# Kernel optimization log

Hardware: AMD Instinct MI355X
Metric: run time of the kernel (lower is better)

The kernel has to match this reference:

```python
import jax, jax.numpy as jnp
import numpy as np

B, C, H, W = 8, 128, 256, 256
D = 64            # embed_dim
S = 32            # max_segments


def setup_inputs() -> dict:
    key = jax.random.key(0)
    ks = jax.random.split(key, 8)
    return {
        "segment_labels": jax.random.randint(ks[0], (B, 1, H, W), 0, S, dtype=jnp.int32),
        "features": jax.random.normal(ks[1], (B, C, H, W), jnp.float32),
        # 1x1 conv stack feat_proj: Conv2d(C->D), ReLU, Conv2d(D->D)
        "conv1_w": jax.random.normal(ks[2], (D, C), jnp.float32) * 0.05,
        "conv1_b": jnp.zeros((D,), jnp.float32),
        "conv2_w": jax.random.normal(ks[3], (D, D), jnp.float32) * 0.1,
        "conv2_b": jnp.zeros((D,), jnp.float32),
        # nn.Embedding(max_segments + 1, embed_dim)
        "embed_table": jax.random.normal(ks[4], (S + 1, D), jnp.float32) * 0.02,
        # nn.Linear(2*D, D): y = x @ W.T + b, W is (out, in)
        "out_w": jax.random.normal(ks[5], (D, 2 * D), jnp.float32) * 0.05,
        "out_b": jnp.zeros((D,), jnp.float32),
    }


def reference(segment_labels, features, conv1_w, conv1_b, conv2_w, conv2_b,
              embed_table, out_w, out_b):
    Bb, Cc, Hh, Ww = features.shape
    P = Hh * Ww
    Smax = embed_table.shape[0] - 1  # max_segments

    # feat_proj: two 1x1 convs == per-pixel GEMMs
    x = features.reshape(Bb, Cc, P)                                   # (B,C,P)
    h1 = jnp.maximum(jnp.einsum('oc,bcp->bpo', conv1_w, x) + conv1_b, 0.0)  # (B,P,D)
    feat = jnp.einsum('od,bpd->bpo', conv2_w, h1) + conv2_b           # (B,P,D)

    # Per-(batch, segment-id) masked mean via a single segment-sum pass.
    labels = segment_labels[:, 0].reshape(Bb, P)                       # (B,P) in [0,S)
    ids = (labels + Smax * jnp.arange(Bb, dtype=labels.dtype)[:, None]).reshape(-1)
    sums = jax.ops.segment_sum(feat.reshape(Bb * P, -1), ids,
                               num_segments=Bb * Smax).reshape(Bb, Smax, -1)
    counts = jax.ops.segment_sum(jnp.ones((Bb * P,), feat.dtype), ids,
                                 num_segments=Bb * Smax).reshape(Bb, Smax)
    pooled = sums / jnp.maximum(counts, 1.0)[..., None]                # (B,S,D) (zeros where absent)

    # type embedding for seg_id s (already in [0,S), clamp is a no-op but faithful)
    type_emb = embed_table[jnp.clip(jnp.arange(Smax), 0, Smax)]        # (S,D)
    combined = jnp.concatenate(
        [pooled, jnp.broadcast_to(type_emb, (Bb, Smax, type_emb.shape[-1]))], axis=-1)
    combined = jnp.einsum('oe,bse->bso', out_w, combined) + out_b      # (B,S,D)

    # torch.unique returns sorted present labels; compact present segments to the
    # front (rank order), pad rest with zeros.
    present = counts > 0                                               # (B,S)
    rank = jnp.cumsum(present.astype(jnp.int32), axis=1) - 1
    dst = jnp.where(present, rank, Smax)                               # Smax = dropped slot
    bidx = jnp.broadcast_to(jnp.arange(Bb)[:, None], (Bb, Smax))
    out = jnp.zeros_like(combined)
    out = out.at[bidx, dst].set(combined, mode='drop')
    return out
```

## Files before the change

kernel.cpp:

```cpp
#include <hip/hip_runtime.h>


#define B_ 8
#define C_ 128
#define P_ 65536
#define D_ 64
#define S_ 32
#define TM 256
#define KC 32
#define NCH (C_ / KC)

typedef short  bf16x8 __attribute__((ext_vector_type(8)));
typedef float  f32x4  __attribute__((ext_vector_type(4)));

__device__ __forceinline__ short f2bf(float f) {
  union { float f; unsigned u; } v; v.f = f;
  unsigned r = v.u + 0x7fffu + ((v.u >> 16) & 1u);
  return (short)(r >> 16);
}

__device__ __forceinline__ void gload16(const float* g, float* l) {
  __builtin_amdgcn_global_load_lds(
      (const __attribute__((address_space(1))) void*)g,
      (__attribute__((address_space(3))) void*)l, 16, 0, 0);
}

__global__ __launch_bounds__(256) void w1_to_bf16(const float* __restrict__ w1,
                                                  short* __restrict__ wbf) {
  int i = blockIdx.x * 256 + threadIdx.x;
  if (i < C_ * D_) wbf[i] = f2bf(w1[i]);
}

__global__ __launch_bounds__(256, 2) void proj_mfma(
    const int* __restrict__ labels, const float* __restrict__ feat,
    const short* __restrict__ wbf, const float* __restrict__ b1,
    float* __restrict__ gsum, int* __restrict__ gcnt)
{
  __shared__ __align__(16) float lds_x[2][KC * TM];
  __shared__ float s_acc[S_][68];
  __shared__ int   s_cnt[S_];

  const int tid  = threadIdx.x;
  const int wave = tid >> 6, l = tid & 63, m = l & 15, g = l >> 4;
  const int b    = blockIdx.y;
  const int px0  = blockIdx.x * TM;

  for (int i = tid; i < S_ * 68; i += 256) ((float*)s_acc)[i] = 0.f;
  if (tid < S_) s_cnt[tid] = 0;
  __syncthreads();

  const float* xb = feat + (size_t)b * C_ * P_ + px0;
  const int lane4 = l * 4;

  #pragma unroll
  for (int i = 0; i < 8; ++i)
    gload16(xb + (size_t)(wave * 8 + i) * P_ + lane4,
            &lds_x[0][(wave * 8 + i) * TM]);

  f32x4 acc[4][4];
  #pragma unroll
  for (int t = 0; t < 4; ++t)
    #pragma unroll
    for (int nt = 0; nt < 4; ++nt) acc[t][nt] = (f32x4){0.f, 0.f, 0.f, 0.f};

  #pragma unroll
  for (int kc = 0; kc < NCH; ++kc) {
    bf16x8 bw[4];
    #pragma unroll
    for (int nt = 0; nt < 4; ++nt)
      bw[nt] = *(const bf16x8*)&wbf[(nt * 16 + m) * C_ + kc * KC + g * 8];

    if (kc + 1 < NCH) {
      #pragma unroll
      for (int i = 0; i < 8; ++i)
        gload16(xb + (size_t)((kc + 1) * KC + wave * 8 + i) * P_ + lane4,
                &lds_x[(kc + 1) & 1][(wave * 8 + i) * TM]);
      asm volatile("s_waitcnt vmcnt(8)" ::: "memory");
    } else {
      asm volatile("s_waitcnt vmcnt(0)" ::: "memory");
    }
    __builtin_amdgcn_s_barrier();
    asm volatile("" ::: "memory");

    const float* bp = lds_x[kc & 1];
    #pragma unroll
    for (int t = 0; t < 4; ++t) {
      const int bpx = wave * 64 + t * 16 + m;
      bf16x8 af;
      #pragma unroll
      for (int j = 0; j < 8; ++j)
        af[j] = f2bf(bp[(g * 8 + j) * TM + bpx]);
      #pragma unroll
      for (int nt = 0; nt < 4; ++nt)
        acc[t][nt] = __builtin_amdgcn_mfma_f32_16x16x32_bf16(af, bw[nt],
                                                             acc[t][nt], 0, 0, 0);
    }
    asm volatile("s_waitcnt lgkmcnt(0)" ::: "memory");
    __builtin_amdgcn_sched_barrier(0);
    __builtin_amdgcn_s_barrier();
  }

  float b1v[4];
  #pragma unroll
  for (int nt = 0; nt < 4; ++nt) b1v[nt] = b1[nt * 16 + m];

  const int* lb = labels + (size_t)b * P_ + px0;
  #pragma unroll
  for (int t = 0; t < 4; ++t) {
    const int4 lv = *(const int4*)&lb[wave * 64 + t * 16 + g * 4];
    #pragma unroll
    for (int nt = 0; nt < 4; ++nt) {
      #pragma unroll
      for (int r = 0; r < 4; ++r) {
        const int lab = ((r & 2) ? ((r & 1) ? lv.w : lv.z)
                                 : ((r & 1) ? lv.y : lv.x)) & (S_ - 1);
        const float v = fmaxf(acc[t][nt][r] + b1v[nt], 0.f);
        atomicAdd(&s_acc[lab][nt * 16 + m], v);
      }
    }
    if (m < 4) {
      const int lab = ((m & 2) ? ((m & 1) ? lv.w : lv.z)
                               : ((m & 1) ? lv.y : lv.x)) & (S_ - 1);
      atomicAdd(&s_cnt[lab], 1);
    }
  }

  __syncthreads();
  for (int i = tid; i < S_ * D_; i += 256)
    atomicAdd(&gsum[(size_t)b * S_ * D_ + i], s_acc[i >> 6][i & 63]);
  if (tid < S_) atomicAdd(&gcnt[b * S_ + tid], s_cnt[tid]);
}

__global__ __launch_bounds__(64) void seg_finalize2(
    const float* __restrict__ gsum, const int* __restrict__ gcnt,
    const float* __restrict__ w2, const float* __restrict__ b2,
    const float* __restrict__ emb, const float* __restrict__ wo,
    const float* __restrict__ bo, float* __restrict__ out)
{
  const int s = blockIdx.x, b = blockIdx.y, o = threadIdx.x;
  const int co = (o < S_) ? gcnt[b * S_ + o] : 0;
  const unsigned long long mask = __ballot(co > 0);
  const int cnt = gcnt[b * S_ + s];
  if (cnt <= 0) return;
  const int rank = __popcll(mask & ((1ull << s) - 1ull));

  __shared__ float s_mean[D_], s_pool[D_];
  s_mean[o] = gsum[((size_t)b * S_ + s) * D_ + o] * (1.f / (float)cnt);
  __syncthreads();
  float pooled = b2[o];
  #pragma unroll
  for (int d = 0; d < D_; ++d) pooled += w2[o * D_ + d] * s_mean[d];
  s_pool[o] = pooled;
  __syncthreads();
  float r = bo[o];
  #pragma unroll
  for (int e = 0; e < D_; ++e) r += wo[o * 2 * D_ + e] * s_pool[e];
  #pragma unroll
  for (int e = 0; e < D_; ++e) r += wo[o * 2 * D_ + D_ + e] * emb[s * D_ + e];
  out[((size_t)b * S_ + rank) * D_ + o] = r;
}

extern "C" void kernel_launch(void* const* d_in, const int* in_sizes, int n_in,
                              void* d_out, int out_size, void* d_ws, size_t ws_size,
                              hipStream_t stream) {
  const int*   labels = (const int*)  d_in[0];
  const float* feat   = (const float*)d_in[1];
  const float* w1     = (const float*)d_in[2];
  const float* b1     = (const float*)d_in[3];
  const float* w2     = (const float*)d_in[4];
  const float* b2     = (const float*)d_in[5];
  const float* emb    = (const float*)d_in[6];
  const float* wo     = (const float*)d_in[7];
  const float* bo     = (const float*)d_in[8];
  float* out = (float*)d_out;

  char* w = (char*)d_ws;
  float* gsum = (float*)w;   w += (size_t)B_ * S_ * D_ * 4;
  int*   gcnt = (int*)w;     w += (size_t)B_ * S_ * 4;
  short* wbf  = (short*)w;

  hipMemsetAsync(d_ws, 0, (size_t)B_ * S_ * D_ * 4 + (size_t)B_ * S_ * 4, stream);
  hipMemsetAsync(d_out, 0, (size_t)out_size * sizeof(float), stream);

  w1_to_bf16<<<(C_ * D_ + 255) / 256, 256, 0, stream>>>(w1, wbf);

  dim3 grid(P_ / TM, B_);
  proj_mfma<<<grid, 256, 0, stream>>>(labels, feat, wbf, b1, gsum, gcnt);
  seg_finalize2<<<dim3(S_, B_), 64, 0, stream>>>(gsum, gcnt, w2, b2, emb, wo, bo, out);
}
```

Before: 233.6 us.

## Load features directly to registers with per-wave double-buffered pipeline and swizzled LDS weights

Replaces the block-wide LDS staging of feature tiles (global_load_lds with barriers) with per-wave direct global-to-register loads, software-pipelined across two register buffers so the next 16-pixel tile is in flight while the current one runs through MFMA. The bf16 weight matrix is staged once into XOR-swizzled LDS instead of being re-read from global memory on every K chunk. Each block now covers 512 pixels, with a higher occupancy hint and no intra-loop barriers. In exchange it uses many more registers (64 floats of prefetch), and each lane's loads are strided 64-byte segments rather than wide 16-byte vectors, which may hurt memory efficiency.

```diff
diff --git a/kernel.cpp b/kernel.cpp
--- a/kernel.cpp
+++ b/kernel.cpp
@@ -6,9 +6,9 @@
 #define P_ 65536
 #define D_ 64
 #define S_ 32
-#define TM 256
-#define KC 32
-#define NCH (C_ / KC)
+#define WPB 4
+#define TMW 128
+#define TMB (WPB * TMW)
 
 typedef short  bf16x8 __attribute__((ext_vector_type(8)));
 typedef float  f32x4  __attribute__((ext_vector_type(4)));
@@ -19,111 +19,98 @@
   return (short)(r >> 16);
 }
 
-__device__ __forceinline__ void gload16(const float* g, float* l) {
-  __builtin_amdgcn_global_load_lds(
-      (const __attribute__((address_space(1))) void*)g,
-      (__attribute__((address_space(3))) void*)l, 16, 0, 0);
-}
-
 __global__ __launch_bounds__(256) void w1_to_bf16(const float* __restrict__ w1,
                                                   short* __restrict__ wbf) {
   int i = blockIdx.x * 256 + threadIdx.x;
   if (i < C_ * D_) wbf[i] = f2bf(w1[i]);
 }
 
-__global__ __launch_bounds__(256, 2) void proj_mfma(
+__global__ __launch_bounds__(256, 4) void proj_mfma(
     const int* __restrict__ labels, const float* __restrict__ feat,
     const short* __restrict__ wbf, const float* __restrict__ b1,
     float* __restrict__ gsum, int* __restrict__ gcnt)
 {
-  __shared__ __align__(16) float lds_x[2][KC * TM];
+  __shared__ __align__(16) char wlds[D_ * 256];
   __shared__ float s_acc[S_][68];
   __shared__ int   s_cnt[S_];
 
   const int tid  = threadIdx.x;
   const int wave = tid >> 6, l = tid & 63, m = l & 15, g = l >> 4;
   const int b    = blockIdx.y;
-  const int px0  = blockIdx.x * TM;
+  const int px0  = blockIdx.x * TMB;
 
+  #pragma unroll
+  for (int i = 0; i < 4; ++i) {
+    const int e = tid * 32 + i * 8;
+    const int row = e >> 7, colB = (e & 127) * 2;
+    *(bf16x8*)&wlds[row * 256 + (colB ^ ((row & 7) << 4))] =
+        *(const bf16x8*)&wbf[e];
+  }
   for (int i = tid; i < S_ * 68; i += 256) ((float*)s_acc)[i] = 0.f;
   if (tid < S_) s_cnt[tid] = 0;
   __syncthreads();
 
-  const float* xb = feat + (size_t)b * C_ * P_ + px0;
-  const int lane4 = l * 4;
-
-  #pragma unroll
-  for (int i = 0; i < 8; ++i)
-    gload16(xb + (size_t)(wave * 8 + i) * P_ + lane4,
-            &lds_x[0][(wave * 8 + i) * TM]);
-
-  f32x4 acc[4][4];
-  #pragma unroll
-  for (int t = 0; t < 4; ++t)
-    #pragma unroll
-    for (int nt = 0; nt < 4; ++nt) acc[t][nt] = (f32x4){0.f, 0.f, 0.f, 0.f};
-
-  #pragma unroll
-  for (int kc = 0; kc < NCH; ++kc) {
-    bf16x8 bw[4];
-    #pragma unroll
-    for (int nt = 0; nt < 4; ++nt)
-      bw[nt] = *(const bf16x8*)&wbf[(nt * 16 + m) * C_ + kc * KC + g * 8];
-
-    if (kc + 1 < NCH) {
-      #pragma unroll
-      for (int i = 0; i < 8; ++i)
-        gload16(xb + (size_t)((kc + 1) * KC + wave * 8 + i) * P_ + lane4,
-                &lds_x[(kc + 1) & 1][(wave * 8 + i) * TM]);
-      asm volatile("s_waitcnt vmcnt(8)" ::: "memory");
-    } else {
-      asm volatile("s_waitcnt vmcnt(0)" ::: "memory");
-    }
-    __builtin_amdgcn_s_barrier();
-    asm volatile("" ::: "memory");
-
-    const float* bp = lds_x[kc & 1];
-    #pragma unroll
-    for (int t = 0; t < 4; ++t) {
-      const int bpx = wave * 64 + t * 16 + m;
-      bf16x8 af;
-      #pragma unroll
-      for (int j = 0; j < 8; ++j)
-        af[j] = f2bf(bp[(g * 8 + j) * TM + bpx]);
-      #pragma unroll
-      for (int nt = 0; nt < 4; ++nt)
-        acc[t][nt] = __builtin_amdgcn_mfma_f32_16x16x32_bf16(af, bw[nt],
-                                                             acc[t][nt], 0, 0, 0);
-    }
-    asm volatile("s_waitcnt lgkmcnt(0)" ::: "memory");
-    __builtin_amdgcn_sched_barrier(0);
-    __builtin_amdgcn_s_barrier();
-  }
+  const float* xpg = feat + (size_t)b * C_ * P_ + (size_t)(g * 8) * P_
+                   + px0 + wave * TMW + m;
+  const int*   lb  = labels + (size_t)b * P_ + px0 + wave * TMW;
+  const int    xsw = (m & 7) << 4;
 
   float b1v[4];
   #pragma unroll
   for (int nt = 0; nt < 4; ++nt) b1v[nt] = b1[nt * 16 + m];
 
-  const int* lb = labels + (size_t)b * P_ + px0;
+  float xvA[4][8], xvB[4][8];
+
+#define ISSUE(dst, t_) do {                                                   \
+    _Pragma("unroll") for (int kk = 0; kk < 4; ++kk)                          \
+    _Pragma("unroll") for (int j = 0; j < 8; ++j)                             \
+      dst[kk][j] = xpg[(size_t)(kk * 32 + j) * P_ + (t_) * 16];               \
+  } while (0)
+
+#define COMPUTE(src, t_) do {                                                 \
+    f32x4 acc[4] = {{0,0,0,0},{0,0,0,0},{0,0,0,0},{0,0,0,0}};                 \
+    _Pragma("unroll") for (int ks = 0; ks < 4; ++ks) {                        \
+      bf16x8 af;                                                              \
+      _Pragma("unroll") for (int j = 0; j < 8; ++j) af[j] = f2bf(src[ks][j]); \
+      _Pragma("unroll") for (int nt = 0; nt < 4; ++nt) {                      \
+        bf16x8 bwv = *(const bf16x8*)&wlds[(nt * 16 + m) * 256 +              \
+                                           ((ks * 64 + g * 16) ^ xsw)];       \
+        acc[nt] = __builtin_amdgcn_mfma_f32_16x16x32_bf16(af, bwv,            \
+                                                          acc[nt], 0, 0, 0);  \
+      }                                                                       \
+    }                                                                         \
+    const int4 lv = *(const int4*)&lb[(t_) * 16 + g * 4];                     \
+    _Pragma("unroll") for (int nt = 0; nt < 4; ++nt)                          \
+      _Pragma("unroll") for (int r = 0; r < 4; ++r) {                         \
+        const int lab = ((r & 2) ? ((r & 1) ? lv.w : lv.z)                    \
+                                 : ((r & 1) ? lv.y : lv.x)) & (S_ - 1);       \
+        atomicAdd(&s_acc[lab][nt * 16 + m],                                   \
+                  fmaxf(acc[nt][r] + b1v[nt], 0.f));                          \
+      }                                                                       \
+    if (m < 4) {                                                              \
+      const int lab = ((m & 2) ? ((m & 1) ? lv.w : lv.z)                      \
+                               : ((m & 1) ? lv.y : lv.x)) & (S_ - 1);         \
+      atomicAdd(&s_cnt[lab], 1);                                              \
+    }                                                                         \
+  } while (0)
+
+  ISSUE(xvA, 0);
+  __builtin_amdgcn_sched_barrier(0);
   #pragma unroll
-  for (int t = 0; t < 4; ++t) {
-    const int4 lv = *(const int4*)&lb[wave * 64 + t * 16 + g * 4];
-    #pragma unroll
-    for (int nt = 0; nt < 4; ++nt) {
-      #pragma unroll
-      for (int r = 0; r < 4; ++r) {
-        const int lab = ((r & 2) ? ((r & 1) ? lv.w : lv.z)
-                                 : ((r & 1) ? lv.y : lv.x)) & (S_ - 1);
-        const float v = fmaxf(acc[t][nt][r] + b1v[nt], 0.f);
-        atomicAdd(&s_acc[lab][nt * 16 + m], v);
-      }
+  for (int t = 0; t < 8; t += 2) {
+    ISSUE(xvB, t + 1);
+    __builtin_amdgcn_sched_barrier(0);
+    COMPUTE(xvA, t);
+    __builtin_amdgcn_sched_barrier(0);
+    if (t + 2 < 8) {
+      ISSUE(xvA, t + 2);
+      __builtin_amdgcn_sched_barrier(0);
     }
-    if (m < 4) {
-      const int lab = ((m & 2) ? ((m & 1) ? lv.w : lv.z)
-                               : ((m & 1) ? lv.y : lv.x)) & (S_ - 1);
-      atomicAdd(&s_cnt[lab], 1);
-    }
+    COMPUTE(xvB, t + 1);
+    __builtin_amdgcn_sched_barrier(0);
   }
+#undef ISSUE
+#undef COMPUTE
 
   __syncthreads();
   for (int i = tid; i < S_ * D_; i += 256)
@@ -184,7 +171,7 @@
 
   w1_to_bf16<<<(C_ * D_ + 255) / 256, 256, 0, stream>>>(w1, wbf);
 
-  dim3 grid(P_ / TM, B_);
+  dim3 grid(P_ / TMB, B_);
   proj_mfma<<<grid, 256, 0, stream>>>(labels, feat, wbf, b1, gsum, gcnt);
   seg_finalize2<<<dim3(S_, B_), 64, 0, stream>>>(gsum, gcnt, w2, b2, emb, wo, bo, out);
 }
```

Result: faster. 203.4 us (-12.9%).

## Replace double buffer with 4-stage padded LDS ring and preload weights

Applied to the files above, without the earlier changes.

The projection kernel's two-slot 32-channel double buffer becomes a four-slot ring of 16-channel stages, with up to four stages in flight and rows padded to 260 floats to reduce LDS bank conflicts. All bf16 weight fragments and biases are loaded into registers once before the loop, and the K loop is fully unrolled into four explicit phases with hand-placed waits and barriers. The goal is deeper prefetch of the memory-bound feature stream and fewer per-chunk weight loads, at the cost of more registers and more fragile hand scheduling.

```diff
diff --git a/kernel.cpp b/kernel.cpp
--- a/kernel.cpp
+++ b/kernel.cpp
@@ -6,12 +6,11 @@
 #define P_ 65536
 #define D_ 64
 #define S_ 32
-#define TM 256
-#define KC 32
-#define NCH (C_ / KC)
-
-typedef short  bf16x8 __attribute__((ext_vector_type(8)));
-typedef float  f32x4  __attribute__((ext_vector_type(4)));
+#define PXT 256
+#define ROWPAD 260
+
+typedef short bf16x8 __attribute__((ext_vector_type(8)));
+typedef float f32x4  __attribute__((ext_vector_type(4)));
 
 __device__ __forceinline__ short f2bf(float f) {
   union { float f; unsigned u; } v; v.f = f;
@@ -19,16 +18,16 @@
   return (short)(r >> 16);
 }
 
-__device__ __forceinline__ void gload16(const float* g, float* l) {
-  __builtin_amdgcn_global_load_lds(
-      (const __attribute__((address_space(1))) void*)g,
-      (__attribute__((address_space(3))) void*)l, 16, 0, 0);
-}
-
 __global__ __launch_bounds__(256) void w1_to_bf16(const float* __restrict__ w1,
                                                   short* __restrict__ wbf) {
   int i = blockIdx.x * 256 + threadIdx.x;
   if (i < C_ * D_) wbf[i] = f2bf(w1[i]);
+}
+
+__device__ __forceinline__ void gload16(const float* g, const float* l) {
+  __builtin_amdgcn_global_load_lds(
+      (const __attribute__((address_space(1))) float*)g,
+      (__attribute__((address_space(3))) float*)l, 16, 0, 0);
 }
 
 __global__ __launch_bounds__(256, 2) void proj_mfma(
@@ -36,86 +35,100 @@
     const short* __restrict__ wbf, const float* __restrict__ b1,
     float* __restrict__ gsum, int* __restrict__ gcnt)
 {
-  __shared__ __align__(16) float lds_x[2][KC * TM];
+  __shared__ __align__(16) float ring[4][16 * ROWPAD];
   __shared__ float s_acc[S_][68];
   __shared__ int   s_cnt[S_];
 
   const int tid  = threadIdx.x;
   const int wave = tid >> 6, l = tid & 63, m = l & 15, g = l >> 4;
   const int b    = blockIdx.y;
-  const int px0  = blockIdx.x * TM;
+  const int px0  = blockIdx.x * PXT;
 
   for (int i = tid; i < S_ * 68; i += 256) ((float*)s_acc)[i] = 0.f;
   if (tid < S_) s_cnt[tid] = 0;
-  __syncthreads();
+
+  bf16x8 bfr[4][4];
+  #pragma unroll
+  for (int nt = 0; nt < 4; ++nt)
+    #pragma unroll
+    for (int u = 0; u < 4; ++u)
+      bfr[nt][u] = *(const bf16x8*)&wbf[(nt * 16 + m) * C_ + u * 32 + g * 8];
+  float b1v[4];
+  #pragma unroll
+  for (int nt = 0; nt < 4; ++nt) b1v[nt] = b1[nt * 16 + m];
 
   const float* xb = feat + (size_t)b * C_ * P_ + px0;
-  const int lane4 = l * 4;
-
-  #pragma unroll
-  for (int i = 0; i < 8; ++i)
-    gload16(xb + (size_t)(wave * 8 + i) * P_ + lane4,
-            &lds_x[0][(wave * 8 + i) * TM]);
+
+#define STAGE(c_) do {                                                        \
+    _Pragma("unroll") for (int i = 0; i < 4; ++i)                             \
+      gload16(xb + (size_t)((c_) * 16 + wave * 4 + i) * P_ + l * 4,           \
+              &ring[(c_) & 3][(wave * 4 + i) * ROWPAD]);                      \
+  } while (0)
+
+#define WAITV(n_) do {                                                        \
+    asm volatile("s_waitcnt vmcnt(" #n_ ")" ::: "memory");                    \
+    __builtin_amdgcn_sched_barrier(0);                                        \
+  } while (0)
+
+#define PAIR(u_) do {                                                         \
+    _Pragma("unroll") for (int v = 0; v < 4; ++v) {                           \
+      const int px = wave * 64 + v * 16 + m;                                  \
+      const float* sl = &ring[(2 * (u_) + (g >> 1)) & 3]                      \
+                             [((g & 1) * 8) * ROWPAD + px];                   \
+      bf16x8 af;                                                              \
+      _Pragma("unroll") for (int j = 0; j < 8; ++j)                           \
+        af[j] = f2bf(sl[j * ROWPAD]);                                         \
+      _Pragma("unroll") for (int nt = 0; nt < 4; ++nt)                        \
+        acc[v][nt] = __builtin_amdgcn_mfma_f32_16x16x32_bf16(                 \
+            af, bfr[nt][u_], acc[v][nt], 0, 0, 0);                            \
+    }                                                                         \
+  } while (0)
+
+  STAGE(0); STAGE(1); STAGE(2); STAGE(3);
 
   f32x4 acc[4][4];
   #pragma unroll
-  for (int t = 0; t < 4; ++t)
+  for (int v = 0; v < 4; ++v)
     #pragma unroll
-    for (int nt = 0; nt < 4; ++nt) acc[t][nt] = (f32x4){0.f, 0.f, 0.f, 0.f};
-
-  #pragma unroll
-  for (int kc = 0; kc < NCH; ++kc) {
-    bf16x8 bw[4];
-    #pragma unroll
-    for (int nt = 0; nt < 4; ++nt)
-      bw[nt] = *(const bf16x8*)&wbf[(nt * 16 + m) * C_ + kc * KC + g * 8];
-
-    if (kc + 1 < NCH) {
-      #pragma unroll
-      for (int i = 0; i < 8; ++i)
-        gload16(xb + (size_t)((kc + 1) * KC + wave * 8 + i) * P_ + lane4,
-                &lds_x[(kc + 1) & 1][(wave * 8 + i) * TM]);
-      asm volatile("s_waitcnt vmcnt(8)" ::: "memory");
-    } else {
-      asm volatile("s_waitcnt vmcnt(0)" ::: "memory");
-    }
-    __builtin_amdgcn_s_barrier();
-    asm volatile("" ::: "memory");
-
-    const float* bp = lds_x[kc & 1];
-    #pragma unroll
-    for (int t = 0; t < 4; ++t) {
-      const int bpx = wave * 64 + t * 16 + m;
-      bf16x8 af;
-      #pragma unroll
-      for (int j = 0; j < 8; ++j)
-        af[j] = f2bf(bp[(g * 8 + j) * TM + bpx]);
-      #pragma unroll
-      for (int nt = 0; nt < 4; ++nt)
-        acc[t][nt] = __builtin_amdgcn_mfma_f32_16x16x32_bf16(af, bw[nt],
-                                                             acc[t][nt], 0, 0, 0);
-    }
-    asm volatile("s_waitcnt lgkmcnt(0)" ::: "memory");
-    __builtin_amdgcn_sched_barrier(0);
-    __builtin_amdgcn_s_barrier();
-  }
-
-  float b1v[4];
-  #pragma unroll
-  for (int nt = 0; nt < 4; ++nt) b1v[nt] = b1[nt * 16 + m];
-
-  const int* lb = labels + (size_t)b * P_ + px0;
-  #pragma unroll
-  for (int t = 0; t < 4; ++t) {
-    const int4 lv = *(const int4*)&lb[wave * 64 + t * 16 + g * 4];
+    for (int nt = 0; nt < 4; ++nt) acc[v][nt] = (f32x4){0.f, 0.f, 0.f, 0.f};
+
+  WAITV(8);
+  __builtin_amdgcn_s_barrier();
+  PAIR(0);
+  __builtin_amdgcn_sched_barrier(0);
+  __builtin_amdgcn_s_barrier();
+  STAGE(4); STAGE(5);
+  WAITV(8);
+  __builtin_amdgcn_s_barrier();
+  PAIR(1);
+  __builtin_amdgcn_sched_barrier(0);
+  __builtin_amdgcn_s_barrier();
+  STAGE(6); STAGE(7);
+  WAITV(8);
+  __builtin_amdgcn_s_barrier();
+  PAIR(2);
+  __builtin_amdgcn_sched_barrier(0);
+  WAITV(0);
+  __builtin_amdgcn_s_barrier();
+  PAIR(3);
+  __builtin_amdgcn_sched_barrier(0);
+
+#undef STAGE
+#undef WAITV
+#undef PAIR
+
+  const int* lb = labels + (size_t)b * P_ + px0 + wave * 64;
+  #pragma unroll
+  for (int v = 0; v < 4; ++v) {
+    const int4 lv = *(const int4*)&lb[v * 16 + g * 4];
     #pragma unroll
     for (int nt = 0; nt < 4; ++nt) {
       #pragma unroll
       for (int r = 0; r < 4; ++r) {
         const int lab = ((r & 2) ? ((r & 1) ? lv.w : lv.z)
                                  : ((r & 1) ? lv.y : lv.x)) & (S_ - 1);
-        const float v = fmaxf(acc[t][nt][r] + b1v[nt], 0.f);
-        atomicAdd(&s_acc[lab][nt * 16 + m], v);
+        atomicAdd(&s_acc[lab][nt * 16 + m],
+                  fmaxf(acc[v][nt][r] + b1v[nt], 0.f));
       }
     }
     if (m < 4) {
@@ -184,7 +197,7 @@
 
   w1_to_bf16<<<(C_ * D_ + 255) / 256, 256, 0, stream>>>(w1, wbf);
 
-  dim3 grid(P_ / TM, B_);
+  dim3 grid(P_ / PXT, B_);
   proj_mfma<<<grid, 256, 0, stream>>>(labels, feat, wbf, b1, gsum, gcnt);
   seg_finalize2<<<dim3(S_, B_), 64, 0, stream>>>(gsum, gcnt, w2, b2, emb, wo, bo, out);
 }
```

Result: no change. 233.0 us (-0.2%).

## Pre-convert features to bf16 and load MFMA operands directly without LDS staging

Applied to the files above, without the earlier changes.

Adds a separate pass that converts the whole fp32 feature tensor to packed bf16 in workspace, then the projection kernel reads bf16 pairs straight from global memory into MFMA A-fragments instead of staging fp32 through double-buffered LDS. Each wave now owns 128 pixels processed as two interleaved 16-pixel tiles, with all W1 fragments held in registers, and occupancy hint is raised to 4. The extra conversion pass reads 256MB and writes 128MB, so total traffic rises. The direct strided global loads may also be less coalesced than the earlier LDS path.

```diff
diff --git a/kernel.cpp b/kernel.cpp
--- a/kernel.cpp
+++ b/kernel.cpp
@@ -6,24 +6,15 @@
 #define P_ 65536
 #define D_ 64
 #define S_ 32
-#define TM 256
-#define KC 32
-#define NCH (C_ / KC)
 
-typedef short  bf16x8 __attribute__((ext_vector_type(8)));
-typedef float  f32x4  __attribute__((ext_vector_type(4)));
+typedef short bf16x8 __attribute__((ext_vector_type(8)));
+typedef float f32x4  __attribute__((ext_vector_type(4)));
 
-__device__ __forceinline__ short f2bf(float f) {
+__device__ __forceinline__ unsigned f2bfu(float f) {
   union { float f; unsigned u; } v; v.f = f;
-  unsigned r = v.u + 0x7fffu + ((v.u >> 16) & 1u);
-  return (short)(r >> 16);
+  return (v.u + 0x7fffu + ((v.u >> 16) & 1u)) >> 16;
 }
-
-__device__ __forceinline__ void gload16(const float* g, float* l) {
-  __builtin_amdgcn_global_load_lds(
-      (const __attribute__((address_space(1))) void*)g,
-      (__attribute__((address_space(3))) void*)l, 16, 0, 0);
-}
+__device__ __forceinline__ short f2bf(float f) { return (short)f2bfu(f); }
 
 __global__ __launch_bounds__(256) void w1_to_bf16(const float* __restrict__ w1,
                                                   short* __restrict__ wbf) {
@@ -31,97 +22,103 @@
   if (i < C_ * D_) wbf[i] = f2bf(w1[i]);
 }
 
-__global__ __launch_bounds__(256, 2) void proj_mfma(
-    const int* __restrict__ labels, const float* __restrict__ feat,
-    const short* __restrict__ wbf, const float* __restrict__ b1,
-    float* __restrict__ gsum, int* __restrict__ gcnt)
+__global__ __launch_bounds__(256) void feat_to_bf16(const float4* __restrict__ in,
+                                                    uint4* __restrict__ out) {
+  const int n = (B_ * C_ * P_) / 8;
+  const int stride = gridDim.x * 256;
+  for (int i = blockIdx.x * 256 + threadIdx.x; i < n; i += stride) {
+    const float4 a = in[2 * i], b = in[2 * i + 1];
+    uint4 o;
+    o.x = f2bfu(a.x) | (f2bfu(a.y) << 16);
+    o.y = f2bfu(a.z) | (f2bfu(a.w) << 16);
+    o.z = f2bfu(b.x) | (f2bfu(b.y) << 16);
+    o.w = f2bfu(b.z) | (f2bfu(b.w) << 16);
+    out[i] = o;
+  }
+}
+
+template<bool PACKED>
+__global__ __launch_bounds__(256, 4) void proj_mfma(
+    const int* __restrict__ labels, const float* __restrict__ featf,
+    const unsigned* __restrict__ featb, const short* __restrict__ wbf,
+    const float* __restrict__ b1, float* __restrict__ gsum,
+    int* __restrict__ gcnt)
 {
-  __shared__ __align__(16) float lds_x[2][KC * TM];
   __shared__ float s_acc[S_][68];
   __shared__ int   s_cnt[S_];
 
-  const int tid  = threadIdx.x;
+  const int tid = threadIdx.x;
   const int wave = tid >> 6, l = tid & 63, m = l & 15, g = l >> 4;
-  const int b    = blockIdx.y;
-  const int px0  = blockIdx.x * TM;
+  const int b   = blockIdx.y;
+  const int px0 = blockIdx.x * 512 + wave * 128;
 
   for (int i = tid; i < S_ * 68; i += 256) ((float*)s_acc)[i] = 0.f;
   if (tid < S_) s_cnt[tid] = 0;
   __syncthreads();
 
-  const float* xb = feat + (size_t)b * C_ * P_ + px0;
-  const int lane4 = l * 4;
-
+  bf16x8 bfr[4][4];
   #pragma unroll
-  for (int i = 0; i < 8; ++i)
-    gload16(xb + (size_t)(wave * 8 + i) * P_ + lane4,
-            &lds_x[0][(wave * 8 + i) * TM]);
-
-  f32x4 acc[4][4];
-  #pragma unroll
-  for (int t = 0; t < 4; ++t)
+  for (int nt = 0; nt < 4; ++nt)
     #pragma unroll
-    for (int nt = 0; nt < 4; ++nt) acc[t][nt] = (f32x4){0.f, 0.f, 0.f, 0.f};
-
-  #pragma unroll
-  for (int kc = 0; kc < NCH; ++kc) {
-    bf16x8 bw[4];
-    #pragma unroll
-    for (int nt = 0; nt < 4; ++nt)
-      bw[nt] = *(const bf16x8*)&wbf[(nt * 16 + m) * C_ + kc * KC + g * 8];
-
-    if (kc + 1 < NCH) {
-      #pragma unroll
-      for (int i = 0; i < 8; ++i)
-        gload16(xb + (size_t)((kc + 1) * KC + wave * 8 + i) * P_ + lane4,
-                &lds_x[(kc + 1) & 1][(wave * 8 + i) * TM]);
-      asm volatile("s_waitcnt vmcnt(8)" ::: "memory");
-    } else {
-      asm volatile("s_waitcnt vmcnt(0)" ::: "memory");
-    }
-    __builtin_amdgcn_s_barrier();
-    asm volatile("" ::: "memory");
-
-    const float* bp = lds_x[kc & 1];
-    #pragma unroll
-    for (int t = 0; t < 4; ++t) {
-      const int bpx = wave * 64 + t * 16 + m;
-      bf16x8 af;
-      #pragma unroll
-      for (int j = 0; j < 8; ++j)
-        af[j] = f2bf(bp[(g * 8 + j) * TM + bpx]);
-      #pragma unroll
-      for (int nt = 0; nt < 4; ++nt)
-        acc[t][nt] = __builtin_amdgcn_mfma_f32_16x16x32_bf16(af, bw[nt],
-                                                             acc[t][nt], 0, 0, 0);
-    }
-    asm volatile("s_waitcnt lgkmcnt(0)" ::: "memory");
-    __builtin_amdgcn_sched_barrier(0);
-    __builtin_amdgcn_s_barrier();
-  }
-
+    for (int ks = 0; ks < 4; ++ks)
+      bfr[nt][ks] = *(const bf16x8*)&wbf[(nt * 16 + m) * C_ + ks * 32 + g * 8];
   float b1v[4];
   #pragma unroll
   for (int nt = 0; nt < 4; ++nt) b1v[nt] = b1[nt * 16 + m];
 
-  const int* lb = labels + (size_t)b * P_ + px0;
-  #pragma unroll
-  for (int t = 0; t < 4; ++t) {
-    const int4 lv = *(const int4*)&lb[wave * 64 + t * 16 + g * 4];
+  const int* lb = labels + (size_t)b * P_;
+
+  for (int it = 0; it < 4; ++it) {
+    const int pp = px0 + it * 32;
+    f32x4 aA[4], aB[4];
     #pragma unroll
     for (int nt = 0; nt < 4; ++nt) {
+      aA[nt] = (f32x4){0.f, 0.f, 0.f, 0.f};
+      aB[nt] = (f32x4){0.f, 0.f, 0.f, 0.f};
+    }
+
+    #pragma unroll
+    for (int ks = 0; ks < 4; ++ks) {
+      bf16x8 afA, afB;
+      if (PACKED) {
+        const unsigned* xp = featb
+            + ((size_t)b * C_ + ks * 32 + g * 8) * (P_ / 2) + (pp >> 1) + m;
+        #pragma unroll
+        for (int j = 0; j < 8; ++j) {
+          const unsigned v = xp[(size_t)j * (P_ / 2)];
+          afA[j] = (short)(v & 0xffffu);
+          afB[j] = (short)(v >> 16);
+        }
+      } else {
+        const float* xp = featf
+            + ((size_t)b * C_ + ks * 32 + g * 8) * P_ + pp + 2 * m;
+        #pragma unroll
+        for (int j = 0; j < 8; ++j) {
+          afA[j] = f2bf(xp[(size_t)j * P_]);
+          afB[j] = f2bf(xp[(size_t)j * P_ + 1]);
+        }
+      }
       #pragma unroll
-      for (int r = 0; r < 4; ++r) {
-        const int lab = ((r & 2) ? ((r & 1) ? lv.w : lv.z)
-                                 : ((r & 1) ? lv.y : lv.x)) & (S_ - 1);
-        const float v = fmaxf(acc[t][nt][r] + b1v[nt], 0.f);
-        atomicAdd(&s_acc[lab][nt * 16 + m], v);
+      for (int nt = 0; nt < 4; ++nt) {
+        aA[nt] = __builtin_amdgcn_mfma_f32_16x16x32_bf16(afA, bfr[nt][ks], aA[nt], 0, 0, 0);
+        aB[nt] = __builtin_amdgcn_mfma_f32_16x16x32_bf16(afB, bfr[nt][ks], aB[nt], 0, 0, 0);
+      }
+    }
+
+    #pragma unroll
+    for (int r = 0; r < 4; ++r) {
+      const int2 lv = *(const int2*)&lb[pp + 2 * (g * 4 + r)];
+      const int lA = lv.x & (S_ - 1), lB = lv.y & (S_ - 1);
+      #pragma unroll
+      for (int nt = 0; nt < 4; ++nt) {
+        atomicAdd(&s_acc[lA][nt * 16 + m], fmaxf(aA[nt][r] + b1v[nt], 0.f));
+        atomicAdd(&s_acc[lB][nt * 16 + m], fmaxf(aB[nt][r] + b1v[nt], 0.f));
       }
     }
     if (m < 4) {
-      const int lab = ((m & 2) ? ((m & 1) ? lv.w : lv.z)
-                               : ((m & 1) ? lv.y : lv.x)) & (S_ - 1);
-      atomicAdd(&s_cnt[lab], 1);
+      const int2 lv = *(const int2*)&lb[pp + 2 * (g * 4 + m)];
+      atomicAdd(&s_cnt[lv.x & (S_ - 1)], 1);
+      atomicAdd(&s_cnt[lv.y & (S_ - 1)], 1);
     }
   }
 
@@ -175,16 +172,23 @@
   float* out = (float*)d_out;
 
   char* w = (char*)d_ws;
-  float* gsum = (float*)w;   w += (size_t)B_ * S_ * D_ * 4;
-  int*   gcnt = (int*)w;     w += (size_t)B_ * S_ * 4;
-  short* wbf  = (short*)w;
+  float*    gsum = (float*)w;    w += (size_t)B_ * S_ * D_ * 4;
+  int*      gcnt = (int*)w;      w += (size_t)B_ * S_ * 4;
+  short*    wbf  = (short*)w;    w += (size_t)C_ * D_ * 2;
+  unsigned* xbf  = (unsigned*)w; w += (size_t)B_ * C_ * P_ * 2;
+  const bool packed = ((size_t)(w - (char*)d_ws) <= ws_size);
 
   hipMemsetAsync(d_ws, 0, (size_t)B_ * S_ * D_ * 4 + (size_t)B_ * S_ * 4, stream);
   hipMemsetAsync(d_out, 0, (size_t)out_size * sizeof(float), stream);
 
   w1_to_bf16<<<(C_ * D_ + 255) / 256, 256, 0, stream>>>(w1, wbf);
 
-  dim3 grid(P_ / TM, B_);
-  proj_mfma<<<grid, 256, 0, stream>>>(labels, feat, wbf, b1, gsum, gcnt);
+  dim3 grid(P_ / 512, B_);
+  if (packed) {
+    feat_to_bf16<<<2048, 256, 0, stream>>>((const float4*)feat, (uint4*)xbf);
+    proj_mfma<true><<<grid, 256, 0, stream>>>(labels, feat, xbf, wbf, b1, gsum, gcnt);
+  } else {
+    proj_mfma<false><<<grid, 256, 0, stream>>>(labels, feat, xbf, wbf, b1, gsum, gcnt);
+  }
   seg_finalize2<<<dim3(S_, B_), 64, 0, stream>>>(gsum, gcnt, w2, b2, emb, wo, bo, out);
 }
```

New measurement: 268.2 us. 1.15x slower.
